# Optimization experiments

Measured on AMD Instinct MI355X. Metric: run time of the kernel, lower is better.

Reference implementation:

```python
import jax, jax.numpy as jnp
import numpy as np

B, T, N, F_IN, F_OUT, H = 32, 32, 256, 32, 32, 256
NEG_SLOPE = 0.2  # GATConv default leaky-relu slope


def setup_inputs() -> dict:
    key = jax.random.key(0)
    ks = jax.random.split(key, 12)
    x = jax.random.normal(ks[0], (B, T, N, F_IN), dtype=jnp.float32)
    u = jax.random.uniform(ks[1], (B, T, N, N))
    w = jax.random.uniform(ks[2], (B, T, N, N))
    adj = jnp.where(u < 0.1, w, 0.0).astype(jnp.float32)
    # GAT params (heads=1, concat=False)
    W = jax.random.normal(ks[3], (F_IN, F_OUT), dtype=jnp.float32) / np.sqrt(F_IN)
    a_src = jax.random.normal(ks[4], (F_OUT,), dtype=jnp.float32) / np.sqrt(F_OUT)
    a_dst = jax.random.normal(ks[5], (F_OUT,), dtype=jnp.float32) / np.sqrt(F_OUT)
    gat_b = jnp.zeros((F_OUT,), dtype=jnp.float32)
    # LSTM params (PyTorch layout, gate order i,f,g,o)
    IN = N * F_OUT
    s = 1.0 / np.sqrt(H)
    W_ih = jax.random.uniform(ks[6], (4 * H, IN), minval=-s, maxval=s, dtype=jnp.float32)
    W_hh = jax.random.uniform(ks[7], (4 * H, H), minval=-s, maxval=s, dtype=jnp.float32)
    b_ih = jax.random.uniform(ks[8], (4 * H,), minval=-s, maxval=s, dtype=jnp.float32)
    b_hh = jax.random.uniform(ks[9], (4 * H,), minval=-s, maxval=s, dtype=jnp.float32)
    # output Linear
    Wo = jax.random.uniform(ks[10], (N, H), minval=-s, maxval=s, dtype=jnp.float32)
    bo = jax.random.uniform(ks[11], (N,), minval=-s, maxval=s, dtype=jnp.float32)
    return {"x": x, "adj": adj, "W": W, "a_src": a_src, "a_dst": a_dst,
            "gat_b": gat_b, "W_ih": W_ih, "W_hh": W_hh, "b_ih": b_ih,
            "b_hh": b_hh, "Wo": Wo, "bo": bo}


def _gat(x, adj, W, a_src, a_dst, gat_b):
    # batched over (B,T). h: [B,T,N,F_OUT]
    h = jnp.einsum('btnf,fo->btno', x, W)
    s_src = jnp.einsum('btno,o->btn', h, a_src)  # contribution of source node j
    s_dst = jnp.einsum('btno,o->btn', h, a_dst)  # contribution of target node i
    # e[i,j] = LeakyReLU(a_dst.h_i + a_src.h_j)
    e = jax.nn.leaky_relu(s_dst[..., :, None] + s_src[..., None, :], NEG_SLOPE)
    # edge (row=j -> col=i) exists iff adj[j,i] != 0; GATConv adds self-loops
    mask = (jnp.swapaxes(adj, -1, -2) != 0) | jnp.eye(N, dtype=bool)
    alpha = jax.nn.softmax(jnp.where(mask, e, -jnp.inf), axis=-1)  # softmax over sources j per target i
    return jnp.einsum('btij,btjo->btio', alpha, h) + gat_b


def _lstm_last(seq, W_ih, W_hh, b_ih, b_hh):
    # seq: [B,T,IN] -> last hidden state [B,H]
    def step(carry, x_t):
        h_prev, c_prev = carry
        gates = x_t @ W_ih.T + h_prev @ W_hh.T + (b_ih + b_hh)
        i, f, g, o = jnp.split(gates, 4, axis=-1)
        c = jax.nn.sigmoid(f) * c_prev + jax.nn.sigmoid(i) * jnp.tanh(g)
        h = jax.nn.sigmoid(o) * jnp.tanh(c)
        return (h, c), None
    init = (jnp.zeros((seq.shape[0], H), seq.dtype), jnp.zeros((seq.shape[0], H), seq.dtype))
    (h_last, _), _ = jax.lax.scan(step, init, jnp.swapaxes(seq, 0, 1))
    return h_last


def reference(x, adj, W, a_src, a_dst, gat_b, W_ih, W_hh, b_ih, b_hh, Wo, bo):
    gat_out = _gat(x, adj, W, a_src, a_dst, gat_b)            # [B,T,N,F_OUT]
    seq = gat_out.reshape(gat_out.shape[0], gat_out.shape[1], -1)  # [B,T,N*F_OUT]
    h_last = _lstm_last(seq, W_ih, W_hh, b_ih, b_hh)          # [B,H]
    return h_last @ Wo.T + bo                                  # [B,N]
```

## Files before the change

kernel.cpp:

```cpp
#include <hip/hip_runtime.h>
#include <cstdint>

constexpr int B_ = 32, T_ = 32, N_ = 256, FIN = 32, FOUT = 32, H_ = 256;
constexpr int IN_ = N_ * FOUT;
constexpr int G4  = 4 * H_;
constexpr int BT  = B_ * T_;
constexpr int KZ  = 8;
constexpr int NPACK = 4100;
#define NEG_SLOPE 0.2f

typedef _Float16 half8 __attribute__((ext_vector_type(8)));
typedef _Float16 h2    __attribute__((ext_vector_type(2)));
typedef float    f4    __attribute__((ext_vector_type(4)));

union U48 { uint4 u; half8 h; };

__device__ inline uint32_t pkh2(float a, float b) {
    union { uint32_t u; _Float16 h[2]; } z;
    z.h[0] = (_Float16)a; z.h[1] = (_Float16)b; return z.u;
}
__device__ inline float f16lo(uint32_t u){ union{uint32_t u; _Float16 h[2];} z; z.u=u; return (float)z.h[0]; }
__device__ inline float f16hi(uint32_t u){ union{uint32_t u; _Float16 h[2];} z; z.u=u; return (float)z.h[1]; }

__device__ inline float dot2f(uint32_t w, uint32_t h, float acc) {
    union { uint32_t u; h2 v; } a, b; a.u = w; b.u = h;
#if __has_builtin(__builtin_amdgcn_fdot2)
    return __builtin_amdgcn_fdot2(a.v, b.v, acc, false);
#else
    return acc + (float)a.v.x * (float)b.v.x + (float)a.v.y * (float)b.v.y;
#endif
}

__device__ inline void gload16(const void* g, void* l) {
    __builtin_amdgcn_global_load_lds(
        (const __attribute__((address_space(1))) void*)g,
        (__attribute__((address_space(3))) void*)l, 16, 0, 0);
}

__global__ __launch_bounds__(256) void gat_pack_kernel(
    const float* __restrict__ x, const float* __restrict__ adj,
    const float* __restrict__ W, const float* __restrict__ a_src,
    const float* __restrict__ a_dst, const float* __restrict__ gat_b,
    _Float16* __restrict__ seq,
    const float* __restrict__ Wih, const float* __restrict__ Whh,
    _Float16* __restrict__ wih_h, uint32_t* __restrict__ pwv,
    uint32_t* __restrict__ pwl, uint32_t* __restrict__ pws)
{
    if (blockIdx.x < NPACK) {
        if (blockIdx.x < 4096) {
            int idx = (blockIdx.x * 256 + threadIdx.x) * 8;
            float4 v0 = *reinterpret_cast<const float4*>(Wih + idx);
            float4 v1 = *reinterpret_cast<const float4*>(Wih + idx + 4);
            half8 o;
            o[0]=(_Float16)v0.x; o[1]=(_Float16)v0.y; o[2]=(_Float16)v0.z; o[3]=(_Float16)v0.w;
            o[4]=(_Float16)v1.x; o[5]=(_Float16)v1.y; o[6]=(_Float16)v1.z; o[7]=(_Float16)v1.w;
            *reinterpret_cast<half8*>(wih_h + idx) = o;
        } else {
            int g = (blockIdx.x - 4096) * 256 + threadIdx.x;
            const float* row = Whh + (size_t)g * H_;
            #pragma unroll
            for (int p = 0; p < 128; ++p) {
                float2 v = *reinterpret_cast<const float2*>(row + 2*p);
                uint32_t u = pkh2(v.x, v.y);
                if (p < 64) pwv[p * 1024 + g] = u;
                else if (p < 96) { int pp = p - 64; pwl[(pp >> 2) * 4096 + g * 4 + (pp & 3)] = u; }
                else             { int pp = p - 96; pws[(pp >> 2) * 4096 + g * 4 + (pp & 3)] = u; }
            }
        }
        return;
    }

    const int bt = blockIdx.x - NPACK;
    const int i  = threadIdx.x;
    const int L  = i & 63, w = i >> 6;
    __shared__ float Ws[FIN * FOUT];
    __shared__ __align__(16) _Float16 hT[32 * 264];
    __shared__ __align__(16) uint32_t Pc[256 * 20];
    __shared__ float ssrc[N_];
    __shared__ float linv[N_];
    __shared__ float asv[FOUT], adv[FOUT], gbv[FOUT];

    for (int t = i; t < FIN * FOUT; t += 256) Ws[t] = W[t];
    if (i < FOUT) { asv[i] = a_src[i]; adv[i] = a_dst[i]; gbv[i] = gat_b[i]; }

    float xr[FIN];
    const float* xrow = x + ((size_t)bt * N_ + i) * FIN;
    #pragma unroll
    for (int f4i = 0; f4i < FIN / 4; ++f4i) {
        float4 v = reinterpret_cast<const float4*>(xrow)[f4i];
        xr[4*f4i] = v.x; xr[4*f4i+1] = v.y; xr[4*f4i+2] = v.z; xr[4*f4i+3] = v.w;
    }
    __syncthreads();

    float hr[FOUT];
    #pragma unroll
    for (int k4 = 0; k4 < FOUT / 4; ++k4) {
        float ax = 0.f, ay = 0.f, az = 0.f, aw = 0.f;
        #pragma unroll
        for (int f = 0; f < FIN; ++f) {
            float4 w4 = *reinterpret_cast<const float4*>(&Ws[f*FOUT + 4*k4]);
            ax += xr[f]*w4.x; ay += xr[f]*w4.y; az += xr[f]*w4.z; aw += xr[f]*w4.w;
        }
        hr[4*k4] = ax; hr[4*k4+1] = ay; hr[4*k4+2] = az; hr[4*k4+3] = aw;
    }
    float ss = 0.f, sd = 0.f;
    #pragma unroll
    for (int k = 0; k < FOUT; ++k) { ss += hr[k]*asv[k]; sd += hr[k]*adv[k]; }
    #pragma unroll
    for (int k = 0; k < FOUT; ++k) hT[k*264 + i] = (_Float16)hr[k];
    ssrc[i] = ss;
    __syncthreads();

    float l = 0.f;
    f4 acc[4][2] = {};
    const float* adjcol = adj + (size_t)bt * N_ * N_ + i;
    const int key = (i >> 3) & 3;
    const int m = L & 15, G = L >> 4;

    for (int c = 0; c < 8; ++c) {
        const int j0 = c * 32;
        #pragma unroll
        for (int q = 0; q < 16; ++q) {
            int ja = j0 + 2*q, jb = ja + 1;
            float a0 = adjcol[(size_t)ja * N_];
            float a1 = adjcol[(size_t)jb * N_];
            float e0 = sd + ssrc[ja]; e0 = e0 > 0.f ? e0 : NEG_SLOPE * e0;
            float e1 = sd + ssrc[jb]; e1 = e1 > 0.f ? e1 : NEG_SLOPE * e1;
            float p0 = ((a0 != 0.f) || (ja == i)) ? __expf(e0) : 0.f;
            float p1 = ((a1 != 0.f) || (jb == i)) ? __expf(e1) : 0.f;
            l += p0 + p1;
            Pc[i*20 + (((q >> 2) ^ key) << 2) + (q & 3)] = pkh2(p0, p1);
        }
        U48 b0, b1;
        b0.h = *reinterpret_cast<const half8*>(&hT[m*264      + j0 + G*8]);
        b1.h = *reinterpret_cast<const half8*>(&hT[(m+16)*264 + j0 + G*8]);
        #pragma unroll
        for (int it = 0; it < 4; ++it) {
            int row = w*64 + it*16 + m;
            int rkey = (row >> 3) & 3;
            U48 a;
            a.u = reinterpret_cast<const uint4*>(&Pc[row*20])[G ^ rkey];
            acc[it][0] = __builtin_amdgcn_mfma_f32_16x16x32_f16(a.h, b0.h, acc[it][0], 0, 0, 0);
            acc[it][1] = __builtin_amdgcn_mfma_f32_16x16x32_f16(a.h, b1.h, acc[it][1], 0, 0, 0);
        }
    }
    linv[i] = 1.f / l;
    _Float16* obase = seq + (size_t)bt * IN_;
    #pragma unroll
    for (int it = 0; it < 4; ++it) {
        int ib = w*64 + it*16 + G*4;
        #pragma unroll
        for (int ot = 0; ot < 2; ++ot) {
            int o = ot*16 + m;
            float gb = gbv[o];
            #pragma unroll
            for (int r = 0; r < 4; ++r) {
                int row = ib + r;
                obase[row * FOUT + o] = (_Float16)(acc[it][ot][r] * linv[row] + gb);
            }
        }
    }
}

__global__ __launch_bounds__(256, 4) void gemm_kernel(
    const _Float16* __restrict__ A, const _Float16* __restrict__ Bh,
    float* __restrict__ Gp)
{
    __shared__ __align__(16) _Float16 As[128 * 32];
    __shared__ __align__(16) _Float16 Bs[128 * 32];
    const int t = threadIdx.x;
    const int L = t & 63, w = t >> 6;
    const int wm = w & 1, wn = w >> 1;
    const int m0 = blockIdx.y * 128, n0 = blockIdx.x * 128;
    const int kz = blockIdx.z * 1024;

    f4 acc[4][4] = {};
    const int q0 = t, q1 = t + 256;
    const int row0 = q0 >> 2, kc0 = q0 & 3;
    const int row1 = q1 >> 2, kc1 = q1 & 3;
    const int la = (L & 15) * 32 + (L >> 4) * 8;

    const _Float16* A0 = A + (size_t)(m0 + row0) * IN_ + kz + kc0 * 8;
    const _Float16* A1 = A + (size_t)(m0 + row1) * IN_ + kz + kc1 * 8;
    const _Float16* B0 = Bh + (size_t)(n0 + row0) * IN_ + kz + kc0 * 8;
    const _Float16* B1 = Bh + (size_t)(n0 + row1) * IN_ + kz + kc1 * 8;
    for (int kb = 0; kb < 1024; kb += 32) {
        __syncthreads();
        gload16(A0 + kb, &As[q0 * 8]);
        gload16(A1 + kb, &As[q1 * 8]);
        gload16(B0 + kb, &Bs[q0 * 8]);
        gload16(B1 + kb, &Bs[q1 * 8]);
        __syncthreads();
        half8 af[4], bf[4];
        #pragma unroll
        for (int mi = 0; mi < 4; ++mi)
            af[mi] = *reinterpret_cast<const half8*>(&As[(wm*64 + mi*16) * 32 + la]);
        #pragma unroll
        for (int ni = 0; ni < 4; ++ni)
            bf[ni] = *reinterpret_cast<const half8*>(&Bs[(wn*64 + ni*16) * 32 + la]);
        #pragma unroll
        for (int mi = 0; mi < 4; ++mi)
            #pragma unroll
            for (int ni = 0; ni < 4; ++ni)
                acc[mi][ni] = __builtin_amdgcn_mfma_f32_16x16x32_f16(
                    af[mi], bf[ni], acc[mi][ni], 0, 0, 0);
    }
    float* Gz = Gp + (size_t)blockIdx.z * BT * G4;
    const int cn = n0 + wn * 64 + (L & 15);
    const int rm = m0 + wm * 64 + (L >> 4) * 4;
    #pragma unroll
    for (int mi = 0; mi < 4; ++mi)
        #pragma unroll
        for (int ni = 0; ni < 4; ++ni)
            #pragma unroll
            for (int r = 0; r < 4; ++r)
                Gz[(size_t)(rm + mi*16 + r) * G4 + cn + ni*16] = acc[mi][ni][r];
}

__global__ __launch_bounds__(1024) void lstm_kernel(
    const float* __restrict__ Gp, const uint32_t* __restrict__ pwv,
    const uint32_t* __restrict__ pwl, const uint32_t* __restrict__ pws,
    const float* __restrict__ b_ih, const float* __restrict__ b_hh,
    const float* __restrict__ Wo, const float* __restrict__ bo,
    float* __restrict__ out)
{
    const int b = blockIdx.x;
    const int g = threadIdx.x;
    __shared__ __align__(16) uint32_t hsp[128];
    __shared__ float gsh[G4];
    __shared__ __align__(16) uint32_t wl[8 * 4096];

    uint32_t wv[64];
    #pragma unroll
    for (int p = 0; p < 64; ++p) wv[p] = pwv[p * 1024 + g];
    {
        const uint4* s = reinterpret_cast<const uint4*>(pwl);
        uint4* d = reinterpret_cast<uint4*>(wl);
        #pragma unroll
        for (int r = 0; r < 8; ++r) d[r * 1024 + g] = s[r * 1024 + g];
    }
    if (g < 128) hsp[g] = 0u;
    float c = 0.f;
    const float bias = b_ih[g] + b_hh[g];
    const size_t zs = (size_t)BT * G4;
    const float* Gb = Gp + (size_t)b * T_ * G4 + g;
    const uint4* pws4 = reinterpret_cast<const uint4*>(pws);
    const uint4* wl4  = reinterpret_cast<const uint4*>(wl);
    const uint4* hsp4 = reinterpret_cast<const uint4*>(hsp);

    float gcur = 0.f;
    #pragma unroll
    for (int z = 0; z < KZ; ++z) gcur += Gb[z * zs];
    __syncthreads();

    for (int t = 0; t < T_; ++t) {
        float acc = bias + gcur;
        float pf[KZ];
        const int tn = (t + 1 < T_) ? t + 1 : t;
        #pragma unroll
        for (int z = 0; z < KZ; ++z) pf[z] = Gb[(size_t)tn * G4 + z * zs];
        #pragma unroll
        for (int q = 0; q < 32; ++q) {
            uint4 h4 = hsp4[q];
            uint4 w4;
            if (q < 16) {
                w4.x = wv[4*q]; w4.y = wv[4*q+1]; w4.z = wv[4*q+2]; w4.w = wv[4*q+3];
            } else if (q < 24) {
                w4 = wl4[(q - 16) * 1024 + g];
            } else {
                w4 = pws4[(q - 24) * 1024 + g];
            }
            acc = dot2f(w4.x, h4.x, acc);
            acc = dot2f(w4.y, h4.y, acc);
            acc = dot2f(w4.z, h4.z, acc);
            acc = dot2f(w4.w, h4.w, acc);
        }
        gcur = ((pf[0]+pf[1]) + (pf[2]+pf[3])) + ((pf[4]+pf[5]) + (pf[6]+pf[7]));
        gsh[g] = acc;
        __syncthreads();
        if (g < H_) {
            float xi = gsh[g], xf = gsh[H_ + g], xg = gsh[2*H_ + g], xo = gsh[3*H_ + g];
            float si = 1.f / (1.f + __expf(-xi));
            float sf = 1.f / (1.f + __expf(-xf));
            float so = 1.f / (1.f + __expf(-xo));
            float eg = __expf(2.f * xg);
            float tg = 1.f - 2.f / (eg + 1.f);
            c = sf * c + si * tg;
            float ec = __expf(2.f * c);
            float th = 1.f - 2.f / (ec + 1.f);
            reinterpret_cast<_Float16*>(hsp)[g] = (_Float16)(so * th);
        }
        __syncthreads();
    }
    if (g < N_) {
        const float* worow = Wo + (size_t)g * H_;
        float o = bo[g];
        #pragma unroll
        for (int q = 0; q < 32; ++q) {
            uint4 hq = hsp4[q];
            float4 w0 = *reinterpret_cast<const float4*>(worow + q*8);
            float4 w1 = *reinterpret_cast<const float4*>(worow + q*8 + 4);
            o += w0.x * f16lo(hq.x) + w0.y * f16hi(hq.x)
               + w0.z * f16lo(hq.y) + w0.w * f16hi(hq.y)
               + w1.x * f16lo(hq.z) + w1.y * f16hi(hq.z)
               + w1.z * f16lo(hq.w) + w1.w * f16hi(hq.w);
        }
        out[(size_t)b * N_ + g] = o;
    }
}

extern "C" void kernel_launch(void* const* d_in, const int* in_sizes, int n_in,
                              void* d_out, int out_size, void* d_ws, size_t ws_size,
                              hipStream_t stream) {
    const float* x     = (const float*)d_in[0];
    const float* adj   = (const float*)d_in[1];
    const float* W     = (const float*)d_in[2];
    const float* a_src = (const float*)d_in[3];
    const float* a_dst = (const float*)d_in[4];
    const float* gat_b = (const float*)d_in[5];
    const float* W_ih  = (const float*)d_in[6];
    const float* W_hh  = (const float*)d_in[7];
    const float* b_ih  = (const float*)d_in[8];
    const float* b_hh  = (const float*)d_in[9];
    const float* Wo    = (const float*)d_in[10];
    const float* bo    = (const float*)d_in[11];
    float* out = (float*)d_out;

    _Float16* seq   = (_Float16*)d_ws;
    _Float16* wih_h = seq + (size_t)BT * IN_;
    float*    Gp    = (float*)(wih_h + (size_t)G4 * IN_);
    uint32_t* pwv   = (uint32_t*)(Gp + (size_t)KZ * BT * G4);
    uint32_t* pwl   = pwv + 64 * 1024;
    uint32_t* pws   = pwl + 32 * 1024;

    gat_pack_kernel<<<dim3(NPACK + BT), dim3(256), 0, stream>>>(
        x, adj, W, a_src, a_dst, gat_b, seq, W_ih, W_hh, wih_h, pwv, pwl, pws);
    gemm_kernel<<<dim3(8, 8, KZ), dim3(256), 0, stream>>>(seq, wih_h, Gp);
    lstm_kernel<<<dim3(B_), dim3(1024), 0, stream>>>(Gp, pwv, pwl, pws, b_ih, b_hh, Wo, bo, out);
}
```

Before: 553.8 us.

## Prefetch adjacency columns, double split-K, and schedule GAT blocks before pack blocks

The GAT part of the fused kernel now loads each 32-row chunk of the adjacency column into registers one iteration ahead, so the next chunk's global loads overlap the current chunk's exp and MFMA work. The block order is swapped so the GAT blocks are dispatched first and the weight-packing blocks come last. The input-projection GEMM split-K factor goes from 8 to 16, giving 1024 blocks instead of 512 for better occupancy, and the LSTM sums 16 partials. In exchange this raises register pressure in the GAT kernel and doubles the partial-sum buffer traffic and workspace size.

New measurement: 590.2 us. 6.6% more time.

```diff
diff --git a/kernel.cpp b/kernel.cpp
--- a/kernel.cpp
+++ b/kernel.cpp
@@ -5,7 +5,7 @@
 constexpr int IN_ = N_ * FOUT;
 constexpr int G4  = 4 * H_;
 constexpr int BT  = B_ * T_;
-constexpr int KZ  = 8;
+constexpr int KZ  = 16;
 constexpr int NPACK = 4100;
 #define NEG_SLOPE 0.2f
 
@@ -46,9 +46,10 @@
     _Float16* __restrict__ wih_h, uint32_t* __restrict__ pwv,
     uint32_t* __restrict__ pwl, uint32_t* __restrict__ pws)
 {
-    if (blockIdx.x < NPACK) {
-        if (blockIdx.x < 4096) {
-            int idx = (blockIdx.x * 256 + threadIdx.x) * 8;
+    if (blockIdx.x >= BT) {
+        const int pid = blockIdx.x - BT;
+        if (pid < 4096) {
+            int idx = (pid * 256 + threadIdx.x) * 8;
             float4 v0 = *reinterpret_cast<const float4*>(Wih + idx);
             float4 v1 = *reinterpret_cast<const float4*>(Wih + idx + 4);
             half8 o;
@@ -56,7 +57,7 @@
             o[4]=(_Float16)v1.x; o[5]=(_Float16)v1.y; o[6]=(_Float16)v1.z; o[7]=(_Float16)v1.w;
             *reinterpret_cast<half8*>(wih_h + idx) = o;
         } else {
-            int g = (blockIdx.x - 4096) * 256 + threadIdx.x;
+            int g = (pid - 4096) * 256 + threadIdx.x;
             const float* row = Whh + (size_t)g * H_;
             #pragma unroll
             for (int p = 0; p < 128; ++p) {
@@ -70,7 +71,7 @@
         return;
     }
 
-    const int bt = blockIdx.x - NPACK;
+    const int bt = blockIdx.x;
     const int i  = threadIdx.x;
     const int L  = i & 63, w = i >> 6;
     __shared__ float Ws[FIN * FOUT];
@@ -90,6 +91,10 @@
         float4 v = reinterpret_cast<const float4*>(xrow)[f4i];
         xr[4*f4i] = v.x; xr[4*f4i+1] = v.y; xr[4*f4i+2] = v.z; xr[4*f4i+3] = v.w;
     }
+    const float* adjcol = adj + (size_t)bt * N_ * N_ + i;
+    float va[32];
+    #pragma unroll
+    for (int u = 0; u < 32; ++u) va[u] = adjcol[(size_t)u * N_];
     __syncthreads();
 
     float hr[FOUT];
@@ -113,21 +118,25 @@
 
     float l = 0.f;
     f4 acc[4][2] = {};
-    const float* adjcol = adj + (size_t)bt * N_ * N_ + i;
     const int key = (i >> 3) & 3;
     const int m = L & 15, G = L >> 4;
 
+    #pragma unroll
     for (int c = 0; c < 8; ++c) {
+        float vb[32];
+        if (c < 7) {
+            const int jn = (c + 1) * 32;
+            #pragma unroll
+            for (int u = 0; u < 32; ++u) vb[u] = adjcol[(size_t)(jn + u) * N_];
+        }
         const int j0 = c * 32;
         #pragma unroll
         for (int q = 0; q < 16; ++q) {
             int ja = j0 + 2*q, jb = ja + 1;
-            float a0 = adjcol[(size_t)ja * N_];
-            float a1 = adjcol[(size_t)jb * N_];
             float e0 = sd + ssrc[ja]; e0 = e0 > 0.f ? e0 : NEG_SLOPE * e0;
             float e1 = sd + ssrc[jb]; e1 = e1 > 0.f ? e1 : NEG_SLOPE * e1;
-            float p0 = ((a0 != 0.f) || (ja == i)) ? __expf(e0) : 0.f;
-            float p1 = ((a1 != 0.f) || (jb == i)) ? __expf(e1) : 0.f;
+            float p0 = ((va[2*q] != 0.f)   || (ja == i)) ? __expf(e0) : 0.f;
+            float p1 = ((va[2*q+1] != 0.f) || (jb == i)) ? __expf(e1) : 0.f;
             l += p0 + p1;
             Pc[i*20 + (((q >> 2) ^ key) << 2) + (q & 3)] = pkh2(p0, p1);
         }
@@ -142,6 +151,10 @@
             a.u = reinterpret_cast<const uint4*>(&Pc[row*20])[G ^ rkey];
             acc[it][0] = __builtin_amdgcn_mfma_f32_16x16x32_f16(a.h, b0.h, acc[it][0], 0, 0, 0);
             acc[it][1] = __builtin_amdgcn_mfma_f32_16x16x32_f16(a.h, b1.h, acc[it][1], 0, 0, 0);
+        }
+        if (c < 7) {
+            #pragma unroll
+            for (int u = 0; u < 32; ++u) va[u] = vb[u];
         }
     }
     linv[i] = 1.f / l;
@@ -172,7 +185,7 @@
     const int L = t & 63, w = t >> 6;
     const int wm = w & 1, wn = w >> 1;
     const int m0 = blockIdx.y * 128, n0 = blockIdx.x * 128;
-    const int kz = blockIdx.z * 1024;
+    const int kz = blockIdx.z * (IN_ / KZ);
 
     f4 acc[4][4] = {};
     const int q0 = t, q1 = t + 256;
@@ -184,7 +197,7 @@
     const _Float16* A1 = A + (size_t)(m0 + row1) * IN_ + kz + kc1 * 8;
     const _Float16* B0 = Bh + (size_t)(n0 + row0) * IN_ + kz + kc0 * 8;
     const _Float16* B1 = Bh + (size_t)(n0 + row1) * IN_ + kz + kc1 * 8;
-    for (int kb = 0; kb < 1024; kb += 32) {
+    for (int kb = 0; kb < IN_ / KZ; kb += 32) {
         __syncthreads();
         gload16(A0 + kb, &As[q0 * 8]);
         gload16(A1 + kb, &As[q1 * 8]);
@@ -275,7 +288,13 @@
             acc = dot2f(w4.z, h4.z, acc);
             acc = dot2f(w4.w, h4.w, acc);
         }
-        gcur = ((pf[0]+pf[1]) + (pf[2]+pf[3])) + ((pf[4]+pf[5]) + (pf[6]+pf[7]));
+        {
+            float s01 = pf[0]+pf[1],   s23 = pf[2]+pf[3];
+            float s45 = pf[4]+pf[5],   s67 = pf[6]+pf[7];
+            float s89 = pf[8]+pf[9],   sab = pf[10]+pf[11];
+            float scd = pf[12]+pf[13], sef = pf[14]+pf[15];
+            gcur = ((s01+s23) + (s45+s67)) + ((s89+sab) + (scd+sef));
+        }
         gsh[g] = acc;
         __syncthreads();
         if (g < H_) {
@@ -333,7 +352,7 @@
     uint32_t* pwl   = pwv + 64 * 1024;
     uint32_t* pws   = pwl + 32 * 1024;
 
-    gat_pack_kernel<<<dim3(NPACK + BT), dim3(256), 0, stream>>>(
+    gat_pack_kernel<<<dim3(BT + NPACK), dim3(256), 0, stream>>>(
         x, adj, W, a_src, a_dst, gat_b, seq, W_ih, W_hh, wih_h, pwv, pwl, pws);
     gemm_kernel<<<dim3(8, 8, KZ), dim3(256), 0, stream>>>(seq, wih_h, Gp);
     lstm_kernel<<<dim3(B_), dim3(1024), 0, stream>>>(Gp, pwv, pwl, pws, b_ih, b_hh, Wo, bo, out);
```
